# Kernel optimization log

Measured on AMD Instinct MI355X. Metric: run time of the kernel, lower is better.

The kernel has to match this reference:

```python
import jax, jax.numpy as jnp
import numpy as np
from jax.lax import associative_scan

B, S, D, F, G = 4, 4096, 1024, 4096, 32
EPS = 1e-6


def setup_inputs() -> dict:
    key = jax.random.key(0)
    ks = jax.random.split(key, 16)
    xn = lambda k, shp: jax.random.normal(k, shp, jnp.float32) / np.sqrt(shp[0])
    return {
        "x": jax.random.normal(ks[0], (B, S, D), jnp.float32),
        "Wq": xn(ks[1], (D, D)),
        "Wk": xn(ks[2], (D, D)),
        "Wv": xn(ks[3], (D, D)),
        "Wa": xn(ks[4], (D, 2 * D)),
        "Wg": xn(ks[5], (D, D)),
        "Wo": xn(ks[6], (D, D)),
        "gn_scale": jnp.ones((D,), jnp.float32),
        "gn_bias": jnp.zeros((D,), jnp.float32),
        "ln1_scale": jnp.ones((D,), jnp.float32),
        "ln1_bias": jnp.zeros((D,), jnp.float32),
        "W1": xn(ks[7], (D, F)),
        "b1": jax.random.normal(ks[8], (F,), jnp.float32) * 1e-6,
        "W2": xn(ks[9], (F, D)),
        "b2": jax.random.normal(ks[10], (D,), jnp.float32) * 1e-6,
        "ln2_scale": jnp.ones((D,), jnp.float32),
        "ln2_bias": jnp.zeros((D,), jnp.float32),
    }


def _gate_loop(k, v, q, a):
    # max-headed GateLoop: per-channel complex linear recurrence
    # h_t = a_t * h_{t-1} + k_t * v_t ; y_t = q_t * h_t
    kv = (k * v).astype(jnp.complex64)
    def op(e1, e2):
        a1, x1 = e1
        a2, x2 = e2
        return (a1 * a2, a2 * x1 + x2)
    _, h = associative_scan(op, (a, kv), axis=1)
    return q.astype(jnp.complex64) * h


def _layernorm(x, scale, bias):
    mu = jnp.mean(x, axis=-1, keepdims=True)
    var = jnp.mean(jnp.square(x - mu), axis=-1, keepdims=True)
    return (x - mu) * jax.lax.rsqrt(var + EPS) * scale + bias


def _groupnorm_complex(y, scale, bias):
    # flax GroupNorm on complex input: mean is complex, var = E|y|^2 - |E y|^2 (real)
    b, s, d = y.shape
    yr = y.reshape(b, s, G, d // G)
    mean = jnp.mean(yr, axis=(1, 3), keepdims=True)
    mean2 = jnp.mean(yr.real ** 2 + yr.imag ** 2, axis=(1, 3), keepdims=True)
    var = mean2 - (mean.real ** 2 + mean.imag ** 2)
    yn = (yr - mean) * jax.lax.rsqrt(var + EPS)
    return yn.reshape(b, s, d) * scale + bias


def reference(x, Wq, Wk, Wv, Wa, Wg, Wo, gn_scale, gn_bias, ln1_scale, ln1_bias,
              W1, b1, W2, b2, ln2_scale, ln2_bias):
    q = x @ Wq
    k = x @ Wk
    v = x @ Wv
    a = x @ Wa
    a_real, a_imag = jnp.split(a, 2, axis=-1)
    a_c = a_real + 1j * a_imag
    mag = jnp.abs(a_c)
    phase = jnp.angle(a_c)
    a_c = jax.nn.sigmoid(mag) * jnp.exp(1j * phase)

    g = (x @ Wg).astype(jnp.complex64)

    y = _gate_loop(k, v, q, a_c)                       # [B,S,D] complex64
    y = _groupnorm_complex(y, gn_scale, gn_bias)
    silu_g = g / (1.0 + jnp.exp(-g))                    # complex silu
    y = y * silu_g
    y = (y @ Wo.astype(jnp.complex64)).real

    x = _layernorm(x + y, ln1_scale, ln1_bias)
    h = jax.nn.gelu(x @ W1 + b1)
    out = x + (h @ W2 + b2)
    return _layernorm(out, ln2_scale, ln2_bias)
```

## Files before the change

kernel.cpp:

```cpp
#include <hip/hip_runtime.h>
#include <cstdint>
#include <cstddef>


#define EPSN 1e-6f

typedef _Float16 f16;
typedef _Float16 f16x8 __attribute__((ext_vector_type(8)));
typedef _Float16 f16x4 __attribute__((ext_vector_type(4)));
typedef float    f32x4 __attribute__((ext_vector_type(4)));

static constexpr int    Bb     = 4;
static constexpr int    Ss     = 4096;
static constexpr int    Dd     = 1024;
static constexpr int    Ff     = 4096;
static constexpr int    Mrows  = Bb * Ss;
static constexpr size_t MD     = (size_t)Mrows * Dd;
static constexpr int    CHUNKS = 64;
static constexpr int    CLEN   = Ss / CHUNKS;
static constexpr int    BD     = Bb * Dd;
static constexpr int    CBD    = CHUNKS * BD;
static constexpr size_t MiB    = 1024 * 1024;
static constexpr int    PLD    = 4096;

__device__ __forceinline__ float fast_sigmoid(float x) {
    float e = __builtin_amdgcn_exp2f(-1.4426950408889634f * x);
    return __builtin_amdgcn_rcpf(1.0f + e);
}
__device__ __forceinline__ float gelu_tanh(float x) {
    float z = 0.7978845608028654f * (x + 0.044715f * x * x * x);
    z = fminf(fmaxf(z, -10.0f), 10.0f);
    float e = __builtin_amdgcn_exp2f(2.885390081777927f * z);
    float t = (e - 1.0f) * __builtin_amdgcn_rcpf(e + 1.0f);
    return 0.5f * x * (1.0f + t);
}

__device__ __forceinline__ void async16(const void* g, void* l) {
    __builtin_amdgcn_global_load_lds(
        (const __attribute__((address_space(1))) unsigned int*)(uintptr_t)g,
        (__attribute__((address_space(3))) unsigned int*)(uintptr_t)l,
        16, 0, 0);
}

template <int EPI, typename TC>
__global__ __launch_bounds__(256) void mgemm_k(const f16* __restrict__ A, int lda,
                                               const f16* __restrict__ Bt,
                                               TC* __restrict__ C, int ldc,
                                               int M, int N, int K,
                                               const float* __restrict__ bias) {
    __shared__ f16 As[2][128 * 32];
    __shared__ f16 Bs[2][128 * 32];
    const int tid  = threadIdx.x;
    const int wave = tid >> 6;
    const int lane = tid & 63;

    const int gx  = gridDim.x;
    const int nwg = gx * gridDim.y;
    int bid = blockIdx.y * gx + blockIdx.x;
    bid = (bid & 7) * (nwg >> 3) + (bid >> 3);
    const int bm = (bid / gx) * 128;
    const int bn = (bid % gx) * 128;

    const int rw = (wave & 1) * 64;
    const int cw = (wave >> 1) * 64;

    const int swzc = (((lane & 3) ^ (lane >> 3)) & 3) * 8;
    const f16* gA = A  + (size_t)(bm + wave * 32 + (lane >> 2)) * lda + swzc;
    const f16* gB = Bt + (size_t)(bn + wave * 32 + (lane >> 2)) * K   + swzc;
    f16* const lA0 = &As[0][wave * 1024];
    f16* const lA1 = &As[1][wave * 1024];
    f16* const lB0 = &Bs[0][wave * 1024];
    f16* const lB1 = &Bs[1][wave * 1024];

    f32x4 acc[4][4] = {};

    const int fr  = lane & 15;
    const int fco = (((lane >> 4) ^ (lane >> 1)) & 3) * 8;

#define MG_STAGE(KOFF, LA, LB)                                         \
    {                                                                  \
        async16(gA + (KOFF),                     (LA));                \
        async16(gA + 16 * (size_t)lda + (KOFF),  (LA) + 512);          \
        async16(gB + (KOFF),                     (LB));                \
        async16(gB + 16 * (size_t)K + (KOFF),    (LB) + 512);          \
    }

#define MG_COMPUTE(LSA, LSB)                                                   \
    {                                                                          \
        f16x8 af[4], bfr[4];                                                   \
        _Pragma("unroll") for (int i = 0; i < 4; ++i)                          \
            af[i] = *(const f16x8*)&(LSA)[(rw + i * 16 + fr) * 32 + fco];      \
        _Pragma("unroll") for (int j = 0; j < 4; ++j)                          \
            bfr[j] = *(const f16x8*)&(LSB)[(cw + j * 16 + fr) * 32 + fco];     \
        _Pragma("unroll") for (int i = 0; i < 4; ++i)                          \
            _Pragma("unroll") for (int j = 0; j < 4; ++j)                      \
                acc[i][j] = __builtin_amdgcn_mfma_f32_16x16x32_f16(            \
                    af[i], bfr[j], acc[i][j], 0, 0, 0);                        \
    }

    MG_STAGE(0, lA0, lB0);
    for (int k0 = 0; k0 < K; k0 += 64) {
        __syncthreads();
        MG_STAGE(k0 + 32, lA1, lB1);
        MG_COMPUTE(As[0], Bs[0]);
        __syncthreads();
        if (k0 + 64 < K) MG_STAGE(k0 + 64, lA0, lB0);
        MG_COMPUTE(As[1], Bs[1]);
    }
#undef MG_STAGE
#undef MG_COMPUTE

    const int er = (lane >> 4) * 4;
    const int ec = lane & 15;
#pragma unroll
    for (int i = 0; i < 4; ++i) {
#pragma unroll
        for (int j = 0; j < 4; ++j) {
            const int col = bn + cw + j * 16 + ec;
#pragma unroll
            for (int r = 0; r < 4; ++r) {
                const size_t row = (size_t)(bm + rw + i * 16 + er + r);
                float o = acc[i][j][r];
                if (EPI == 1 || EPI == 2) o += bias[col];
                if (EPI == 1) o = gelu_tanh(o);
                if (sizeof(TC) == 4) ((float*)C)[row * ldc + col] = o;
                else                 ((f16*)C)[row * ldc + col] = (f16)o;
            }
        }
    }
}

__global__ __launch_bounds__(256) void wtrans_k(const float* __restrict__ W,
                                                f16* __restrict__ Wt,
                                                int K, int N) {
    __shared__ float t[32][33];
    const int n0 = blockIdx.x * 32, k0 = blockIdx.y * 32;
    const int tx = threadIdx.x & 31, ty = threadIdx.x >> 5;
#pragma unroll
    for (int i = 0; i < 32; i += 8)
        t[ty + i][tx] = W[(size_t)(k0 + ty + i) * N + n0 + tx];
    __syncthreads();
#pragma unroll
    for (int i = 0; i < 32; i += 8)
        Wt[(size_t)(n0 + ty + i) * K + k0 + tx] = (f16)t[tx][ty + i];
}

__global__ __launch_bounds__(256) void f2h_k(const float* __restrict__ x,
                                             f16* __restrict__ xh) {
    size_t i = ((size_t)blockIdx.x * 256 + threadIdx.x) * 4;
    float4 v = *(const float4*)&x[i];
    f16x4 s;
    s.x = (f16)v.x; s.y = (f16)v.y; s.z = (f16)v.z; s.w = (f16)v.w;
    *(f16x4*)&xh[i] = s;
}

__global__ __launch_bounds__(256) void a_transform_k(f16* __restrict__ a2d) {
    size_t gid = (size_t)blockIdx.x * 256 + threadIdx.x;
    int    j8  = (int)(gid & 127) * 8;
    size_t row = gid >> 7;
    f16x8 vr = *(f16x8*)&a2d[row * 2048 + j8];
    f16x8 vi = *(f16x8*)&a2d[row * 2048 + 1024 + j8];
#pragma unroll
    for (int i = 0; i < 8; ++i) {
        float ar = (float)vr[i], ai = (float)vi[i];
        float mag = sqrtf(ar * ar + ai * ai);
        float sg  = fast_sigmoid(mag);
        float re, im;
        if (mag > 1e-30f) { float s = sg * __builtin_amdgcn_rcpf(mag); re = ar * s; im = ai * s; }
        else              { re = sg; im = 0.0f; }
        vr[i] = (f16)re; vi[i] = (f16)im;
    }
    *(f16x8*)&a2d[row * 2048 + j8]        = vr;
    *(f16x8*)&a2d[row * 2048 + 1024 + j8] = vi;
}

__global__ __launch_bounds__(256) void scan_pass1_k(const f16* __restrict__ a2d,
                                                    const f16* __restrict__ P,
                                                    float4* __restrict__ chunk) {
    int tid = blockIdx.x * 256 + threadIdx.x;
    int d   = tid & 1023;
    int t1  = tid >> 10;
    int b   = t1 & 3;
    int c   = t1 >> 2;
    int t0  = c * CLEN;
    int rbase = b * Ss;
    float Are = 1.0f, Aim = 0.0f, Hre = 0.0f, Him = 0.0f;
    for (int t = t0; t < t0 + CLEN; ++t) {
        int r = rbase + t;
        float are = (float)a2d[(size_t)r * 2048 + d];
        float aim = (float)a2d[(size_t)r * 2048 + 1024 + d];
        float kvv = (float)P[(size_t)r * PLD + 1024 + d]
                  * (float)P[(size_t)r * PLD + 2048 + d];
        float hre = are * Hre - aim * Him + kvv;
        float him = are * Him + aim * Hre;
        Hre = hre; Him = him;
        float pre = are * Are - aim * Aim;
        float pim = are * Aim + aim * Are;
        Are = pre; Aim = pim;
    }
    chunk[tid] = make_float4(Are, Aim, Hre, Him);
}

__global__ __launch_bounds__(256) void scan_pass2_k(const float4* __restrict__ chunk,
                                                    float2* __restrict__ carry,
                                                    float* __restrict__ stats) {
    int tid = blockIdx.x * blockDim.x + threadIdx.x;
    if (tid < 512) stats[tid] = 0.0f;
    float hre = 0.0f, him = 0.0f;
    for (int c = 0; c < CHUNKS; ++c) {
        int task = c * BD + tid;
        float4 ch = chunk[task];
        carry[task] = make_float2(hre, him);
        float nre = ch.x * hre - ch.y * him + ch.z;
        float nim = ch.x * him + ch.y * hre + ch.w;
        hre = nre; him = nim;
    }
}

__global__ __launch_bounds__(256) void scan_pass3_k(const f16* __restrict__ a2d,
                                                    f16* __restrict__ P,
                                                    const float2* __restrict__ carry,
                                                    float* __restrict__ stats) {
    int tid = blockIdx.x * 256 + threadIdx.x;
    int d   = tid & 1023;
    int t1  = tid >> 10;
    int b   = t1 & 3;
    int c   = t1 >> 2;
    int t0  = c * CLEN;
    int rbase = b * Ss;
    float2 cr = carry[tid];
    float hre = cr.x, him = cr.y;
    float sre = 0.0f, sim = 0.0f, s2 = 0.0f;
    for (int t = t0; t < t0 + CLEN; ++t) {
        int r = rbase + t;
        float are = (float)a2d[(size_t)r * 2048 + d];
        float aim = (float)a2d[(size_t)r * 2048 + 1024 + d];
        float kvv = (float)P[(size_t)r * PLD + 1024 + d]
                  * (float)P[(size_t)r * PLD + 2048 + d];
        float nre = are * hre - aim * him + kvv;
        float nim = are * him + aim * hre;
        hre = nre; him = nim;
        float qv  = (float)P[(size_t)r * PLD + d];
        float yr_ = qv * hre;
        float yi_ = qv * him;
        P[(size_t)r * PLD + d] = (f16)yr_;
        sre += yr_; sim += yi_; s2 += yr_ * yr_ + yi_ * yi_;
    }
#pragma unroll
    for (int off = 16; off > 0; off >>= 1) {
        sre += __shfl_down(sre, off, 32);
        sim += __shfl_down(sim, off, 32);
        s2  += __shfl_down(s2,  off, 32);
    }
    if ((threadIdx.x & 31) == 0) {
        int idx = (b * 32 + (d >> 5)) * 4;
        atomicAdd(&stats[idx + 0], sre);
        atomicAdd(&stats[idx + 1], sim);
        atomicAdd(&stats[idx + 2], s2);
    }
}

__global__ __launch_bounds__(256) void gn_gate_k(f16* __restrict__ P,
                                                 const float* __restrict__ stats,
                                                 const float* __restrict__ gn_scale,
                                                 const float* __restrict__ gn_bias) {
    size_t gid = (size_t)blockIdx.x * 256 + threadIdx.x;
    int d8  = (int)(gid & 127) * 8;
    int row = (int)(gid >> 7);
    int b   = row >> 12;
    int grp = d8 >> 5;
    const float* st = &stats[(b * 32 + grp) * 4];
    const float invN = 1.0f / 131072.0f;
    float mre = st[0] * invN;
    float mim = st[1] * invN;
    float var = st[2] * invN - mre * mre - mim * mim;
    float rstd = rsqrtf(var + EPSN);
    f16x8 yv = *(f16x8*)&P[(size_t)row * PLD + d8];
    f16x8 gv = *(const f16x8*)&P[(size_t)row * PLD + 3072 + d8];
#pragma unroll
    for (int i = 0; i < 8; ++i) {
        float re = ((float)yv[i] - mre) * rstd * gn_scale[d8 + i] + gn_bias[d8 + i];
        float gx = (float)gv[i];
        yv[i] = (f16)(re * gx * fast_sigmoid(gx));
    }
    *(f16x8*)&P[(size_t)row * PLD + d8] = yv;
}

__device__ __forceinline__ float ldf(const float* p, size_t i) { return p[i]; }
__device__ __forceinline__ float ldf(const f16* p, size_t i)   { return (float)p[i]; }
__device__ __forceinline__ void  stf(float* p, size_t i, float v) { p[i] = v; }
__device__ __forceinline__ void  stf(f16* p, size_t i, float v)   { p[i] = (f16)v; }

__device__ __forceinline__ float block_reduce_sum(float v, float* s4, int tid) {
#pragma unroll
    for (int off = 32; off > 0; off >>= 1) v += __shfl_down(v, off, 64);
    __syncthreads();
    if ((tid & 63) == 0) s4[tid >> 6] = v;
    __syncthreads();
    return s4[0] + s4[1] + s4[2] + s4[3];
}

template <typename TA, typename TB, typename TO>
__global__ __launch_bounds__(256) void ln_k(const TA* __restrict__ a,
                                            const TB* __restrict__ b,
                                            const float* __restrict__ scale,
                                            const float* __restrict__ bias,
                                            TO* __restrict__ out) {
    __shared__ float s4[4];
    int row = blockIdx.x;
    size_t base = (size_t)row * 1024;
    int tid = threadIdx.x;
    float v[4];
    float s = 0.0f;
#pragma unroll
    for (int i = 0; i < 4; ++i) {
        int d = tid + i * 256;
        v[i] = ldf(a, base + d) + ldf(b, base + d);
        s += v[i];
    }
    float mu = block_reduce_sum(s, s4, tid) * (1.0f / 1024.0f);
    float s2 = 0.0f;
#pragma unroll
    for (int i = 0; i < 4; ++i) {
        float dv = v[i] - mu;
        s2 += dv * dv;
    }
    float var = block_reduce_sum(s2, s4, tid) * (1.0f / 1024.0f);
    float rstd = rsqrtf(var + EPSN);
#pragma unroll
    for (int i = 0; i < 4; ++i) {
        int d = tid + i * 256;
        stf(out, base + d, (v[i] - mu) * rstd * scale[d] + bias[d]);
    }
}

extern "C" void kernel_launch(void* const* d_in, const int* in_sizes, int n_in,
                              void* d_out, int out_size, void* d_ws, size_t ws_size,
                              hipStream_t stream) {
    const float* x        = (const float*)d_in[0];
    const float* Wq       = (const float*)d_in[1];
    const float* Wk       = (const float*)d_in[2];
    const float* Wv       = (const float*)d_in[3];
    const float* Wa       = (const float*)d_in[4];
    const float* Wg       = (const float*)d_in[5];
    const float* Wo       = (const float*)d_in[6];
    const float* gn_scale = (const float*)d_in[7];
    const float* gn_bias  = (const float*)d_in[8];
    const float* ln1_s    = (const float*)d_in[9];
    const float* ln1_b    = (const float*)d_in[10];
    const float* W1       = (const float*)d_in[11];
    const float* b1       = (const float*)d_in[12];
    const float* W2       = (const float*)d_in[13];
    const float* b2       = (const float*)d_in[14];
    const float* ln2_s    = (const float*)d_in[15];
    const float* ln2_b    = (const float*)d_in[16];
    float* out = (float*)d_out;

    char* base = (char*)d_ws;
    f16* W1T = (f16*)(base + 0 * MiB);
    f16* W2T = (f16*)(base + 8 * MiB);
    f16* PWT = (f16*)(base + 16 * MiB);
    f16* WoT = (f16*)(base + 24 * MiB);
    f16* WaT = (f16*)(base + 26 * MiB);
    float4* chunk = (float4*)(base + 30 * MiB);
    float2* carry = (float2*)(base + 34 * MiB);
    float*  stats = (float*)(base + 36 * MiB);
    f16* xb  = (f16*)(base + 37 * MiB);
    f16* P   = (f16*)(base + 69 * MiB);
    f16*   ab = (f16*)d_out;
    f16*   yo = (f16*)d_out;
    f16*   x1 = xb;
    f16*   h1 = P;
    float* h2 = (float*)d_out;

    dim3 blk(256);

    f2h_k<<<Mrows, blk, 0, stream>>>(x, xb);
    wtrans_k<<<dim3(128, 32), blk, 0, stream>>>(W1, W1T, Dd, Ff);
    wtrans_k<<<dim3(32, 128), blk, 0, stream>>>(W2, W2T, Ff, Dd);
    wtrans_k<<<dim3(32, 32),  blk, 0, stream>>>(Wq, PWT + 0u * 1048576, Dd, Dd);
    wtrans_k<<<dim3(32, 32),  blk, 0, stream>>>(Wk, PWT + 1u * 1048576, Dd, Dd);
    wtrans_k<<<dim3(32, 32),  blk, 0, stream>>>(Wv, PWT + 2u * 1048576, Dd, Dd);
    wtrans_k<<<dim3(32, 32),  blk, 0, stream>>>(Wg, PWT + 3u * 1048576, Dd, Dd);
    wtrans_k<<<dim3(32, 32),  blk, 0, stream>>>(Wo, WoT, Dd, Dd);
    wtrans_k<<<dim3(64, 32),  blk, 0, stream>>>(Wa, WaT, Dd, 2 * Dd);

    mgemm_k<0, f16><<<dim3(32, 128), blk, 0, stream>>>(xb, Dd, PWT, P, PLD, Mrows, 4096, Dd, nullptr);
    mgemm_k<0, f16><<<dim3(16, 128), blk, 0, stream>>>(xb, Dd, WaT, ab, 2048, Mrows, 2048, Dd, nullptr);

    a_transform_k<<<MD / (256 * 8), blk, 0, stream>>>(ab);

    scan_pass1_k<<<CBD / 256, blk, 0, stream>>>(ab, P, chunk);
    scan_pass2_k<<<BD / 256, blk, 0, stream>>>(chunk, carry, stats);
    scan_pass3_k<<<CBD / 256, blk, 0, stream>>>(ab, P, carry, stats);

    gn_gate_k<<<MD / (256 * 8), blk, 0, stream>>>(P, stats, gn_scale, gn_bias);

    mgemm_k<0, f16><<<dim3(8, 128), blk, 0, stream>>>(P, PLD, WoT, yo, Dd, Mrows, Dd, Dd, nullptr);
    ln_k<float, f16, f16><<<Mrows, blk, 0, stream>>>(x, yo, ln1_s, ln1_b, x1);

    mgemm_k<1, f16  ><<<dim3(32, 128), blk, 0, stream>>>(x1, Dd, W1T, h1, Ff, Mrows, Ff, Dd, b1);
    mgemm_k<2, float><<<dim3(8, 128),  blk, 0, stream>>>(h1, Ff, W2T, h2, Dd, Mrows, Dd, Ff, b2);

    ln_k<f16, float, float><<<Mrows, blk, 0, stream>>>(x1, h2, ln2_s, ln2_b, out);
}
```

Measured before the change: 1.046 ms.

## Widen GEMM tiles to 128x256 with 8 waves and triple-buffered async loads

The shared GEMM kernel moves from 256 threads with 128x128 tiles and double-buffered LDS to 512 threads with 128x256 tiles and a three-stage LDS ring. The async global-to-LDS prefetch now runs two K-steps ahead, gated by explicit vmcnt waits and raw barriers, and s_setprio is raised around the MFMA block. The goal is more data reuse per tile and better overlap of loads with matrix math. In exchange it uses more LDS per block (72 KiB) and launches fewer workgroups, which may lower occupancy and change wave-level balance.

```diff
diff --git a/kernel.cpp b/kernel.cpp
--- a/kernel.cpp
+++ b/kernel.cpp
@@ -43,13 +43,13 @@
 }
 
 template <int EPI, typename TC>
-__global__ __launch_bounds__(256) void mgemm_k(const f16* __restrict__ A, int lda,
-                                               const f16* __restrict__ Bt,
-                                               TC* __restrict__ C, int ldc,
-                                               int M, int N, int K,
-                                               const float* __restrict__ bias) {
-    __shared__ f16 As[2][128 * 32];
-    __shared__ f16 Bs[2][128 * 32];
+__global__ __launch_bounds__(512, 4) void mgemm_k(const f16* __restrict__ A, int lda,
+                                                  const f16* __restrict__ Bt,
+                                                  TC* __restrict__ C, int ldc,
+                                                  int M, int N, int K,
+                                                  const float* __restrict__ bias) {
+    __shared__ f16 sA[3][128 * 32];
+    __shared__ f16 sB[3][256 * 32];
     const int tid  = threadIdx.x;
     const int wave = tid >> 6;
     const int lane = tid & 63;
@@ -59,56 +59,68 @@
     int bid = blockIdx.y * gx + blockIdx.x;
     bid = (bid & 7) * (nwg >> 3) + (bid >> 3);
     const int bm = (bid / gx) * 128;
-    const int bn = (bid % gx) * 128;
-
-    const int rw = (wave & 1) * 64;
-    const int cw = (wave >> 1) * 64;
+    const int bn = (bid % gx) * 256;
+
+    const int rw = (wave >> 2) * 64;
+    const int cw = (wave & 3) * 64;
 
     const int swzc = (((lane & 3) ^ (lane >> 3)) & 3) * 8;
-    const f16* gA = A  + (size_t)(bm + wave * 32 + (lane >> 2)) * lda + swzc;
-    const f16* gB = Bt + (size_t)(bn + wave * 32 + (lane >> 2)) * K   + swzc;
-    f16* const lA0 = &As[0][wave * 1024];
-    f16* const lA1 = &As[1][wave * 1024];
-    f16* const lB0 = &Bs[0][wave * 1024];
-    f16* const lB1 = &Bs[1][wave * 1024];
+    const f16* gS0 = A  + (size_t)(bm + wave * 16 + (lane >> 2)) * lda + swzc;
+    const f16* gS1 = Bt + (size_t)(bn + wave * 16 + (lane >> 2)) * K   + swzc;
+    const f16* gS2 = Bt + (size_t)(bn + 128 + wave * 16 + (lane >> 2)) * K + swzc;
 
     f32x4 acc[4][4] = {};
 
     const int fr  = lane & 15;
     const int fco = (((lane >> 4) ^ (lane >> 1)) & 3) * 8;
 
-#define MG_STAGE(KOFF, LA, LB)                                         \
-    {                                                                  \
-        async16(gA + (KOFF),                     (LA));                \
-        async16(gA + 16 * (size_t)lda + (KOFF),  (LA) + 512);          \
-        async16(gB + (KOFF),                     (LB));                \
-        async16(gB + 16 * (size_t)K + (KOFF),    (LB) + 512);          \
-    }
-
-#define MG_COMPUTE(LSA, LSB)                                                   \
+    const int NT = K >> 5;
+
+    async16(gS0,      &sA[0][wave * 512]);
+    async16(gS1,      &sB[0][wave * 512]);
+    async16(gS2,      &sB[0][(8 + wave) * 512]);
+    async16(gS0 + 32, &sA[1][wave * 512]);
+    async16(gS1 + 32, &sB[1][wave * 512]);
+    async16(gS2 + 32, &sB[1][(8 + wave) * 512]);
+    asm volatile("s_waitcnt vmcnt(3)" ::: "memory");
+    __builtin_amdgcn_s_barrier();
+
+#define MG_PHASE(T, BR, BS)                                                    \
     {                                                                          \
+        const int t_ = (T);                                                    \
         f16x8 af[4], bfr[4];                                                   \
         _Pragma("unroll") for (int i = 0; i < 4; ++i)                          \
-            af[i] = *(const f16x8*)&(LSA)[(rw + i * 16 + fr) * 32 + fco];      \
+            af[i] = *(const f16x8*)&sA[BR][(rw + i * 16 + fr) * 32 + fco];     \
         _Pragma("unroll") for (int j = 0; j < 4; ++j)                          \
-            bfr[j] = *(const f16x8*)&(LSB)[(cw + j * 16 + fr) * 32 + fco];     \
+            bfr[j] = *(const f16x8*)&sB[BR][(cw + j * 16 + fr) * 32 + fco];    \
+        if (t_ + 2 < NT) {                                                     \
+            const int kk = (t_ + 2) * 32;                                      \
+            async16(gS0 + kk, &sA[BS][wave * 512]);                            \
+            async16(gS1 + kk, &sB[BS][wave * 512]);                            \
+            async16(gS2 + kk, &sB[BS][(8 + wave) * 512]);                      \
+            asm volatile("s_waitcnt vmcnt(3)" ::: "memory");                   \
+        } else {                                                               \
+            asm volatile("s_waitcnt vmcnt(0)" ::: "memory");                   \
+        }                                                                      \
+        __builtin_amdgcn_s_barrier();                                          \
+        __builtin_amdgcn_s_setprio(1);                                         \
         _Pragma("unroll") for (int i = 0; i < 4; ++i)                          \
             _Pragma("unroll") for (int j = 0; j < 4; ++j)                      \
                 acc[i][j] = __builtin_amdgcn_mfma_f32_16x16x32_f16(            \
                     af[i], bfr[j], acc[i][j], 0, 0, 0);                        \
-    }
-
-    MG_STAGE(0, lA0, lB0);
-    for (int k0 = 0; k0 < K; k0 += 64) {
-        __syncthreads();
-        MG_STAGE(k0 + 32, lA1, lB1);
-        MG_COMPUTE(As[0], Bs[0]);
-        __syncthreads();
-        if (k0 + 64 < K) MG_STAGE(k0 + 64, lA0, lB0);
-        MG_COMPUTE(As[1], Bs[1]);
-    }
-#undef MG_STAGE
-#undef MG_COMPUTE
+        __builtin_amdgcn_s_setprio(0);                                         \
+        __builtin_amdgcn_s_barrier();                                          \
+    }
+
+    int t = 0;
+    for (; t + 3 <= NT; t += 3) {
+        MG_PHASE(t,     0, 2)
+        MG_PHASE(t + 1, 1, 0)
+        MG_PHASE(t + 2, 2, 1)
+    }
+    if (t     < NT) MG_PHASE(t,     0, 2)
+    if (t + 1 < NT) MG_PHASE(t + 1, 1, 0)
+#undef MG_PHASE
 
     const int er = (lane >> 4) * 4;
     const int ec = lane & 15;
@@ -374,6 +386,7 @@
     float* h2 = (float*)d_out;
 
     dim3 blk(256);
+    dim3 gblk(512);
 
     f2h_k<<<Mrows, blk, 0, stream>>>(x, xb);
     wtrans_k<<<dim3(128, 32), blk, 0, stream>>>(W1, W1T, Dd, Ff);
@@ -385,8 +398,8 @@
     wtrans_k<<<dim3(32, 32),  blk, 0, stream>>>(Wo, WoT, Dd, Dd);
     wtrans_k<<<dim3(64, 32),  blk, 0, stream>>>(Wa, WaT, Dd, 2 * Dd);
 
-    mgemm_k<0, f16><<<dim3(32, 128), blk, 0, stream>>>(xb, Dd, PWT, P, PLD, Mrows, 4096, Dd, nullptr);
-    mgemm_k<0, f16><<<dim3(16, 128), blk, 0, stream>>>(xb, Dd, WaT, ab, 2048, Mrows, 2048, Dd, nullptr);
+    mgemm_k<0, f16><<<dim3(16, 128), gblk, 0, stream>>>(xb, Dd, PWT, P, PLD, Mrows, 4096, Dd, nullptr);
+    mgemm_k<0, f16><<<dim3(8, 128),  gblk, 0, stream>>>(xb, Dd, WaT, ab, 2048, Mrows, 2048, Dd, nullptr);
 
     a_transform_k<<<MD / (256 * 8), blk, 0, stream>>>(ab);
 
@@ -396,11 +409,11 @@
 
     gn_gate_k<<<MD / (256 * 8), blk, 0, stream>>>(P, stats, gn_scale, gn_bias);
 
-    mgemm_k<0, f16><<<dim3(8, 128), blk, 0, stream>>>(P, PLD, WoT, yo, Dd, Mrows, Dd, Dd, nullptr);
+    mgemm_k<0, f16><<<dim3(4, 128), gblk, 0, stream>>>(P, PLD, WoT, yo, Dd, Mrows, Dd, Dd, nullptr);
     ln_k<float, f16, f16><<<Mrows, blk, 0, stream>>>(x, yo, ln1_s, ln1_b, x1);
 
-    mgemm_k<1, f16  ><<<dim3(32, 128), blk, 0, stream>>>(x1, Dd, W1T, h1, Ff, Mrows, Ff, Dd, b1);
-    mgemm_k<2, float><<<dim3(8, 128),  blk, 0, stream>>>(h1, Ff, W2T, h2, Dd, Mrows, Dd, Ff, b2);
+    mgemm_k<1, f16  ><<<dim3(16, 128), gblk, 0, stream>>>(x1, Dd, W1T, h1, Ff, Mrows, Ff, Dd, b1);
+    mgemm_k<2, float><<<dim3(4, 128),  gblk, 0, stream>>>(h1, Ff, W2T, h2, Dd, Mrows, Dd, Ff, b2);
 
     ln_k<f16, float, float><<<Mrows, blk, 0, stream>>>(x1, h2, ln2_s, ln2_b, out);
 }
```

Result: slower. 1.364 ms (+30.4%).
